# Kernel optimization log

Hardware: AMD Instinct MI355X
Metric: run time of the kernel (lower is better)

Reference implementation:

```python
import jax, jax.numpy as jnp
import numpy as np

NUM_LAYERS = 6
D_MODEL = 256
N_HEADS = 8
N_LEVELS = 4
N_POINTS = 4
D_FFN = 1024
HEAD_DIM = D_MODEL // N_HEADS
B = 2
NQ = 1600
SPATIAL = np.array([[64, 64], [32, 32], [16, 16], [8, 8]], dtype=np.int64)  # (H_l, W_l)
LEVEL_START = np.concatenate([[0], np.cumsum(SPATIAL.prod(1))[:-1]]).astype(np.int64)
S_TOTAL = int(SPATIAL.prod(1).sum())  # 5440


def layer_norm(x, g, b, eps=1e-5):
    mu = x.mean(-1, keepdims=True)
    var = ((x - mu) ** 2).mean(-1, keepdims=True)
    return (x - mu) * jax.lax.rsqrt(var + eps) * g + b


def mha(q, k, v, wq, bq, wk, bk, wv, bv, wo, bo):
    # torch nn.MultiheadAttention math (dropout=eval identity)
    Bb, N, d = q.shape
    def proj(x, w, bias):
        return (x @ w.T + bias).reshape(Bb, -1, N_HEADS, HEAD_DIM).transpose(0, 2, 1, 3)
    qh, kh, vh = proj(q, wq, bq), proj(k, wk, bk), proj(v, wv, bv)
    scores = jnp.einsum('bhqd,bhkd->bhqk', qh, kh) / np.float32(np.sqrt(HEAD_DIM))
    attn = jax.nn.softmax(scores, axis=-1)
    out = jnp.einsum('bhqk,bhkd->bhqd', attn, vh).transpose(0, 2, 1, 3).reshape(Bb, N, d)
    return out @ wo.T + bo


def ms_deform_attn(query, ref_points, src, w_off, b_off, w_attn, b_attn, w_val, b_val, w_out, b_out):
    Bb, Nq, d = query.shape
    value = (src @ w_val.T + b_val).reshape(Bb, -1, N_HEADS, HEAD_DIM)  # [B,S,H,D]
    off = (query @ w_off.T + b_off).reshape(Bb, Nq, N_HEADS, N_LEVELS, N_POINTS, 2)
    aw = (query @ w_attn.T + b_attn).reshape(Bb, Nq, N_HEADS, N_LEVELS * N_POINTS)
    aw = jax.nn.softmax(aw, -1).reshape(Bb, Nq, N_HEADS, N_LEVELS, N_POINTS)
    # offset normalizer is (W_l, H_l)
    norm = jnp.asarray(SPATIAL[:, ::-1].copy(), dtype=query.dtype)  # [L,2]
    loc = ref_points[:, :, None, :, None, :] + off / norm[None, None, None, :, None, :]
    out = jnp.zeros((Bb, Nq, N_HEADS, HEAD_DIM), query.dtype)
    for l in range(N_LEVELS):
        Hl, Wl = int(SPATIAL[l, 0]), int(SPATIAL[l, 1])
        s0 = int(LEVEL_START[l])
        v_l = value[:, s0:s0 + Hl * Wl].transpose(0, 2, 1, 3)  # [B,H,S_l,D]
        loc_l = loc[:, :, :, l]  # [B,Nq,H,P,2]
        # grid_sample bilinear, align_corners=False, padding zeros
        x = loc_l[..., 0] * Wl - 0.5
        y = loc_l[..., 1] * Hl - 0.5
        x0 = jnp.floor(x)
        y0 = jnp.floor(y)
        wx1 = x - x0
        wy1 = y - y0
        samp = jnp.zeros((Bb, Nq, N_HEADS, N_POINTS, HEAD_DIM), query.dtype)
        for dy, wy in ((0, 1.0 - wy1), (1, wy1)):
            for dx, wx in ((0, 1.0 - wx1), (1, wx1)):
                xi = x0 + dx
                yi = y0 + dy
                valid = ((xi >= 0) & (xi <= Wl - 1) & (yi >= 0) & (yi <= Hl - 1)).astype(query.dtype)
                xi_c = jnp.clip(xi, 0, Wl - 1).astype(jnp.int32)
                yi_c = jnp.clip(yi, 0, Hl - 1).astype(jnp.int32)
                idx = (yi_c * Wl + xi_c).transpose(0, 2, 1, 3).reshape(Bb, N_HEADS, Nq * N_POINTS)
                g = jnp.take_along_axis(v_l, idx[..., None], axis=2)  # [B,H,Nq*P,D]
                g = g.reshape(Bb, N_HEADS, Nq, N_POINTS, HEAD_DIM).transpose(0, 2, 1, 3, 4)
                samp = samp + g * (wx * wy * valid)[..., None]
        out = out + (samp * aw[:, :, :, l, :, None]).sum(3)
    return out.reshape(Bb, Nq, d) @ w_out.T + b_out


def decoder_forward(tgt, query_pos, reference_points, src, params):
    out = tgt
    for i in range(NUM_LAYERS):
        p = {k: v[i] for k, v in params.items()}
        q = out + query_pos
        t2 = mha(q, q, out, p['sa_w_q'], p['sa_b_q'], p['sa_w_k'], p['sa_b_k'],
                 p['sa_w_v'], p['sa_b_v'], p['sa_w_o'], p['sa_b_o'])
        out = layer_norm(out + t2, p['ln2_g'], p['ln2_b'])
        t2 = ms_deform_attn(out + query_pos, reference_points, src,
                            p['ca_w_off'], p['ca_b_off'], p['ca_w_attn'], p['ca_b_attn'],
                            p['ca_w_val'], p['ca_b_val'], p['ca_w_out'], p['ca_b_out'])
        out = out + t2
        out = layer_norm(out, p['ln1_g'], p['ln1_b'])
        t2 = jax.nn.relu(out @ p['ffn_w1'].T + p['ffn_b1']) @ p['ffn_w2'].T + p['ffn_b2']
        out = layer_norm(out + t2, p['ln3_g'], p['ln3_b'])
    return out


PARAM_NAMES = ['sa_w_q', 'sa_b_q', 'sa_w_k', 'sa_b_k', 'sa_w_v', 'sa_b_v', 'sa_w_o', 'sa_b_o',
               'ln2_g', 'ln2_b',
               'ca_w_off', 'ca_b_off', 'ca_w_attn', 'ca_b_attn', 'ca_w_val', 'ca_b_val',
               'ca_w_out', 'ca_b_out', 'ln1_g', 'ln1_b',
               'ffn_w1', 'ffn_b1', 'ffn_w2', 'ffn_b2', 'ln3_g', 'ln3_b']


def setup_inputs() -> dict:
    key = jax.random.key(0)
    ks = jax.random.split(key, 64)
    d = D_MODEL
    HLP = N_HEADS * N_LEVELS * N_POINTS
    shapes = {
        'sa_w_q': (d, d), 'sa_b_q': (d,), 'sa_w_k': (d, d), 'sa_b_k': (d,),
        'sa_w_v': (d, d), 'sa_b_v': (d,), 'sa_w_o': (d, d), 'sa_b_o': (d,),
        'ca_w_off': (HLP * 2, d), 'ca_b_off': (HLP * 2,),
        'ca_w_attn': (HLP, d), 'ca_b_attn': (HLP,),
        'ca_w_val': (d, d), 'ca_b_val': (d,),
        'ca_w_out': (d, d), 'ca_b_out': (d,),
        'ffn_w1': (D_FFN, d), 'ffn_b1': (D_FFN,),
        'ffn_w2': (d, D_FFN), 'ffn_b2': (D_FFN * 0 + d,) if False else (d,),
    }
    inp = {}
    inp['tgt'] = jax.random.normal(ks[0], (B, NQ, d), jnp.float32)
    inp['query_pos'] = jax.random.normal(ks[1], (B, NQ, d), jnp.float32)
    inp['reference_points'] = jax.random.uniform(ks[2], (B, NQ, N_LEVELS, 2), jnp.float32)
    inp['src'] = jax.random.normal(ks[3], (B, S_TOTAL, d), jnp.float32)
    i = 4
    for name in PARAM_NAMES:
        if name.startswith('ln'):
            if name.endswith('_g'):
                inp[name] = jnp.ones((NUM_LAYERS, d), jnp.float32)
            else:
                inp[name] = jnp.zeros((NUM_LAYERS, d), jnp.float32)
        else:
            shp = (NUM_LAYERS,) + shapes[name]
            inp[name] = jax.random.normal(ks[i], shp, jnp.float32) * 0.02
            i += 1
    inp['src_spatial_shapes'] = jnp.asarray(SPATIAL)
    inp['src_level_start_index'] = jnp.asarray(LEVEL_START)
    return inp


def reference(tgt, query_pos, reference_points, src,
              sa_w_q, sa_b_q, sa_w_k, sa_b_k, sa_w_v, sa_b_v, sa_w_o, sa_b_o,
              ln2_g, ln2_b,
              ca_w_off, ca_b_off, ca_w_attn, ca_b_attn, ca_w_val, ca_b_val,
              ca_w_out, ca_b_out, ln1_g, ln1_b,
              ffn_w1, ffn_b1, ffn_w2, ffn_b2, ln3_g, ln3_b,
              src_spatial_shapes, src_level_start_index):
    params = dict(zip(PARAM_NAMES, (sa_w_q, sa_b_q, sa_w_k, sa_b_k, sa_w_v, sa_b_v, sa_w_o, sa_b_o,
                                    ln2_g, ln2_b, ca_w_off, ca_b_off, ca_w_attn, ca_b_attn,
                                    ca_w_val, ca_b_val, ca_w_out, ca_b_out, ln1_g, ln1_b,
                                    ffn_w1, ffn_b1, ffn_w2, ffn_b2, ln3_g, ln3_b)))
    return decoder_forward(tgt, query_pos, reference_points, src, params)
```

## Files before the change

### kernel.cpp

```cpp
#include <hip/hip_runtime.h>

#define D_MODEL   256
#define NQ        1600
#define BATCH     2
#define NHEAD     8
#define HDIM      32
#define S_TOTAL   5440
#define D_FFN     1024
#define NUM_LAYERS 6

#define M_Q   (BATCH * NQ)
#define M_V   (BATCH * S_TOTAL)
#define ROW_ELEMS ((size_t)M_Q * D_MODEL)

using short8  = __attribute__((ext_vector_type(8))) short;
using floatx4 = __attribute__((ext_vector_type(4))) float;

__device__ __forceinline__ ushort f2bf(float f) {
    union { float f; unsigned u; } x; x.f = f;
    unsigned r = (x.u + 0x7fffu + ((x.u >> 16) & 1u)) >> 16;
    return (ushort)r;
}
__device__ __forceinline__ float bf2f(ushort b) {
    union { unsigned u; float f; } x; x.u = ((unsigned)b) << 16;
    return x.f;
}

struct GSeg {
    const ushort* A;
    const ushort* W;
    const float*  bias;
    void*         C;
    int           ldc;
    int           mode;
    float         scale;
};
struct GArgs { GSeg s[16]; };

__global__ __launch_bounds__(256) void gemm_multi(GArgs args, int M, int K)
{
    const GSeg sg = args.s[blockIdx.y];
    __shared__ ushort Al[64][40];
    __shared__ ushort Bl[64][40];
    const int tid  = threadIdx.x;
    const int bm   = blockIdx.x * 64;
    const int lr   = tid >> 2;
    const int lc   = tid & 3;
    const int wave = tid >> 6;
    const int lane = tid & 63;
    const int mo   = (wave & 1) * 32;
    const int no   = (wave >> 1) * 32;
    const int row16 = lane & 15;
    const int quad  = lane >> 4;

    floatx4 acc[2][2] = {};

    const ushort* aG = sg.A + (size_t)(bm + lr) * K + lc * 8;
    const ushort* wG = sg.W + (size_t)lr * K + lc * 8;

    for (int k0 = 0; k0 < K; k0 += 32) {
        __syncthreads();
        *(short8*)&Al[lr][lc * 8] = *(const short8*)(aG + k0);
        *(short8*)&Bl[lr][lc * 8] = *(const short8*)(wG + k0);
        __syncthreads();
        short8 af0 = *(const short8*)&Al[mo + row16][quad * 8];
        short8 af1 = *(const short8*)&Al[mo + 16 + row16][quad * 8];
        short8 bf0 = *(const short8*)&Bl[no + row16][quad * 8];
        short8 bf1 = *(const short8*)&Bl[no + 16 + row16][quad * 8];
        acc[0][0] = __builtin_amdgcn_mfma_f32_16x16x32_bf16(af0, bf0, acc[0][0], 0, 0, 0);
        acc[0][1] = __builtin_amdgcn_mfma_f32_16x16x32_bf16(af0, bf1, acc[0][1], 0, 0, 0);
        acc[1][0] = __builtin_amdgcn_mfma_f32_16x16x32_bf16(af1, bf0, acc[1][0], 0, 0, 0);
        acc[1][1] = __builtin_amdgcn_mfma_f32_16x16x32_bf16(af1, bf1, acc[1][1], 0, 0, 0);
    }

#pragma unroll
    for (int mi = 0; mi < 2; ++mi)
#pragma unroll
        for (int ni = 0; ni < 2; ++ni) {
            const int col = no + ni * 16 + row16;
            const float bv = sg.bias[col];
            if (sg.mode == 3) {
                const int rowb = bm + mo + mi * 16 + quad * 4;
                const int b    = rowb / NQ;
                const int mloc = rowb - b * NQ;
                ushort4 st;
                st.x = f2bf((acc[mi][ni][0] + bv) * sg.scale);
                st.y = f2bf((acc[mi][ni][1] + bv) * sg.scale);
                st.z = f2bf((acc[mi][ni][2] + bv) * sg.scale);
                st.w = f2bf((acc[mi][ni][3] + bv) * sg.scale);
                *(ushort4*)((ushort*)sg.C + (size_t)b * (256 * NQ) + (size_t)col * NQ + mloc) = st;
            } else {
#pragma unroll
                for (int r = 0; r < 4; ++r) {
                    const int row = bm + mo + mi * 16 + quad * 4 + r;
                    float v = (acc[mi][ni][r] + bv) * sg.scale;
                    if (sg.mode == 0)
                        ((float*)sg.C)[(size_t)row * sg.ldc + col] = v;
                    else if (sg.mode == 1)
                        ((ushort*)sg.C)[(size_t)row * sg.ldc + col] = f2bf(fmaxf(v, 0.f));
                    else
                        ((ushort*)sg.C)[(size_t)row * sg.ldc + col] = f2bf(v);
                }
            }
        }
}

__global__ __launch_bounds__(256) void attn_mfma(const ushort* __restrict__ Qh,
                                                 const ushort* __restrict__ Kh,
                                                 const ushort* __restrict__ Vt,
                                                 ushort* __restrict__ Oh)
{
    const int bh = blockIdx.x;
    const int h  = bh & 7, b = bh >> 3;
    const int qbase = blockIdx.y * 64;
    const int tid  = threadIdx.x;
    const int wave = tid >> 6, lane = tid & 63;
    const int lr   = lane & 15, quad = lane >> 4;

    __shared__ ushort Kl[64][40];
    __shared__ ushort Vl[32][72];
    __shared__ ushort Pl[4][16][72];

    const short8 qf = *(const short8*)(Qh + (size_t)(b * NQ + qbase + wave * 16 + lr) * 256 + h * 32 + quad * 8);

    float mrow[4] = {-1e30f, -1e30f, -1e30f, -1e30f};
    float lsum[4] = {0.f, 0.f, 0.f, 0.f};
    floatx4 accO[2] = {};
    const floatx4 zero = {0.f, 0.f, 0.f, 0.f};

    const int krow = tid >> 2, kchk = tid & 3;
    const int vrow = tid >> 3, vchk = tid & 7;
    const ushort* Kgb = Kh + (size_t)b * NQ * 256 + h * 32;
    const ushort* Vgb = Vt + (size_t)bh * 32 * NQ;

    for (int k0 = 0; k0 < NQ; k0 += 64) {
        __syncthreads();
        *(short8*)&Kl[krow][kchk * 8] = *(const short8*)(Kgb + (size_t)(k0 + krow) * 256 + kchk * 8);
        *(short8*)&Vl[vrow][vchk * 8] = *(const short8*)(Vgb + (size_t)vrow * NQ + k0 + vchk * 8);
        __syncthreads();

        floatx4 s[4];
#pragma unroll
        for (int cb = 0; cb < 4; ++cb) {
            short8 kf = *(const short8*)&Kl[cb * 16 + lr][quad * 8];
            s[cb] = __builtin_amdgcn_mfma_f32_16x16x32_bf16(qf, kf, zero, 0, 0, 0);
        }
        float corr[4];
#pragma unroll
        for (int r = 0; r < 4; ++r) {
            float mx = fmaxf(fmaxf(s[0][r], s[1][r]), fmaxf(s[2][r], s[3][r]));
            mx = fmaxf(mx, __shfl_xor(mx, 1));
            mx = fmaxf(mx, __shfl_xor(mx, 2));
            mx = fmaxf(mx, __shfl_xor(mx, 4));
            mx = fmaxf(mx, __shfl_xor(mx, 8));
            const float mnew = fmaxf(mrow[r], mx);
            corr[r] = __expf(mrow[r] - mnew);
            mrow[r] = mnew;
        }
        float rsum[4] = {0.f, 0.f, 0.f, 0.f};
#pragma unroll
        for (int cb = 0; cb < 4; ++cb)
#pragma unroll
            for (int r = 0; r < 4; ++r) {
                const float p = __expf(s[cb][r] - mrow[r]);
                s[cb][r] = p;
                rsum[r] += p;
            }
#pragma unroll
        for (int r = 0; r < 4; ++r) {
            float t = rsum[r];
            t += __shfl_xor(t, 1);
            t += __shfl_xor(t, 2);
            t += __shfl_xor(t, 4);
            t += __shfl_xor(t, 8);
            lsum[r] = lsum[r] * corr[r] + t;
            accO[0][r] *= corr[r];
            accO[1][r] *= corr[r];
        }
#pragma unroll
        for (int cb = 0; cb < 4; ++cb)
#pragma unroll
            for (int r = 0; r < 4; ++r)
                Pl[wave][quad * 4 + r][cb * 16 + lr] = f2bf(s[cb][r]);
        __syncthreads();
#pragma unroll
        for (int kc = 0; kc < 2; ++kc) {
            short8 pf = *(const short8*)&Pl[wave][lr][kc * 32 + quad * 8];
            short8 v0 = *(const short8*)&Vl[lr][kc * 32 + quad * 8];
            short8 v1 = *(const short8*)&Vl[16 + lr][kc * 32 + quad * 8];
            accO[0] = __builtin_amdgcn_mfma_f32_16x16x32_bf16(pf, v0, accO[0], 0, 0, 0);
            accO[1] = __builtin_amdgcn_mfma_f32_16x16x32_bf16(pf, v1, accO[1], 0, 0, 0);
        }
    }

    ushort* orow = Oh + (size_t)(b * NQ + qbase + wave * 16) * 256 + h * 32;
#pragma unroll
    for (int r = 0; r < 4; ++r) {
        const float inv = 1.f / lsum[r];
        const int q = quad * 4 + r;
        orow[(size_t)q * 256 + lr]      = f2bf(accO[0][r] * inv);
        orow[(size_t)q * 256 + 16 + lr] = f2bf(accO[1][r] * inv);
    }
}

struct CvtSeg { const float* in; ushort* out; int n4; };
struct CvtArgs { CvtSeg seg[11]; };

__global__ __launch_bounds__(256) void convert_kernel(CvtArgs args)
{
    const CvtSeg sg = args.seg[blockIdx.y];
    const int i = blockIdx.x * 256 + threadIdx.x;
    if (i < sg.n4) {
        float4 v = ((const float4*)sg.in)[i];
        ushort4 o;
        o.x = f2bf(v.x); o.y = f2bf(v.y); o.z = f2bf(v.z); o.w = f2bf(v.w);
        ((ushort4*)sg.out)[i] = o;
    }
}

__global__ __launch_bounds__(256) void init_out_kernel(const float* __restrict__ tgt,
                                                       const float* __restrict__ qpos,
                                                       float* __restrict__ out,
                                                       ushort* __restrict__ out_h,
                                                       ushort* __restrict__ qadd_h, int n4)
{
    const int i = blockIdx.x * 256 + threadIdx.x;
    if (i < n4) {
        float4 v = ((const float4*)tgt)[i];
        float4 p = ((const float4*)qpos)[i];
        ((float4*)out)[i] = v;
        ushort4 o, qa;
        o.x = f2bf(v.x); o.y = f2bf(v.y); o.z = f2bf(v.z); o.w = f2bf(v.w);
        qa.x = f2bf(v.x + p.x); qa.y = f2bf(v.y + p.y);
        qa.z = f2bf(v.z + p.z); qa.w = f2bf(v.w + p.w);
        ((ushort4*)out_h)[i] = o;
        ((ushort4*)qadd_h)[i] = qa;
    }
}

__global__ __launch_bounds__(256) void residual_ln_kernel(const float* __restrict__ x,
                                                          const float* __restrict__ t2,
                                                          const float* __restrict__ g,
                                                          const float* __restrict__ bt,
                                                          const float* __restrict__ qpos,
                                                          float* __restrict__ outp,
                                                          ushort* __restrict__ outp_h,
                                                          ushort* __restrict__ qadd_h)
{
    const int row = blockIdx.x;
    const int c = threadIdx.x;
    const size_t idx = (size_t)row * D_MODEL + c;
    float v = x[idx] + t2[idx];

    float s = v, s2 = v * v;
#pragma unroll
    for (int off = 32; off; off >>= 1) {
        s  += __shfl_xor(s,  off);
        s2 += __shfl_xor(s2, off);
    }
    __shared__ float ws[4], ws2[4];
    const int wid = c >> 6;
    if ((c & 63) == 0) { ws[wid] = s; ws2[wid] = s2; }
    __syncthreads();
    const float tot  = ws[0] + ws[1] + ws[2] + ws[3];
    const float tot2 = ws2[0] + ws2[1] + ws2[2] + ws2[3];
    const float mu  = tot * (1.f / 256.f);
    const float var = tot2 * (1.f / 256.f) - mu * mu;
    const float r = (v - mu) * rsqrtf(var + 1e-5f) * g[c] + bt[c];
    outp[idx] = r;
    outp_h[idx] = f2bf(r);
    qadd_h[idx] = f2bf(r + qpos[idx]);
}

__global__ __launch_bounds__(256) void sample_kernel(const ushort* __restrict__ value,
                                                     const float* __restrict__ off,
                                                     const float* __restrict__ aw,
                                                     const float* __restrict__ ref,
                                                     ushort* __restrict__ outp_h)
{
    const int bq = blockIdx.x;
    const int b  = bq / NQ;
    const int h  = threadIdx.x >> 5;
    const int c  = threadIdx.x & 31;

    const float* offrow = off + (size_t)bq * 256 + h * 32;
    const float* awrow  = aw  + (size_t)bq * 128 + h * 16;
    const float* refrow = ref + (size_t)bq * 8;

    float w16[16];
    {
        float mx = -1e30f;
#pragma unroll
        for (int i = 0; i < 16; ++i) { w16[i] = awrow[i]; mx = fmaxf(mx, w16[i]); }
        float sum = 0.f;
#pragma unroll
        for (int i = 0; i < 16; ++i) { w16[i] = __expf(w16[i] - mx); sum += w16[i]; }
        const float inv = 1.f / sum;
#pragma unroll
        for (int i = 0; i < 16; ++i) w16[i] *= inv;
    }

    const int HL[4]  = {64, 32, 16, 8};
    const int WLv[4] = {64, 32, 16, 8};
    const int S0[4]  = {0, 4096, 5120, 5376};

    float acc = 0.f;
#pragma unroll
    for (int l = 0; l < 4; ++l) {
        const int Hl = HL[l], Wl = WLv[l];
        const float rx = refrow[l * 2 + 0];
        const float ry = refrow[l * 2 + 1];
        const size_t lvl_base = ((size_t)b * S_TOTAL + S0[l]);
#pragma unroll
        for (int p = 0; p < 4; ++p) {
            const float ox = offrow[l * 8 + p * 2 + 0];
            const float oy = offrow[l * 8 + p * 2 + 1];
            const float w  = w16[l * 4 + p];
            const float locx = rx + ox / (float)Wl;
            const float locy = ry + oy / (float)Hl;
            const float x = locx * (float)Wl - 0.5f;
            const float y = locy * (float)Hl - 0.5f;
            const float x0f = floorf(x), y0f = floorf(y);
            const float wx1 = x - x0f, wy1 = y - y0f;
            const int x0 = (int)x0f, y0 = (int)y0f;
#pragma unroll
            for (int dy = 0; dy < 2; ++dy) {
                const int yi = y0 + dy;
                const float wy = dy ? wy1 : (1.f - wy1);
                const bool vy = (yi >= 0) && (yi <= Hl - 1);
                const int yc = min(max(yi, 0), Hl - 1);
#pragma unroll
                for (int dx = 0; dx < 2; ++dx) {
                    const int xi = x0 + dx;
                    const float wx = dx ? wx1 : (1.f - wx1);
                    const bool vx = (xi >= 0) && (xi <= Wl - 1);
                    const int xc = min(max(xi, 0), Wl - 1);
                    const float g = bf2f(value[((lvl_base + (size_t)yc * Wl + xc)) * 256 + h * 32 + c]);
                    acc += (vx && vy) ? g * (wx * wy * w) : 0.f;
                }
            }
        }
    }
    outp_h[(size_t)bq * D_MODEL + h * 32 + c] = f2bf(acc);
}

extern "C" void kernel_launch(void* const* d_in, const int* in_sizes, int n_in,
                              void* d_out, int out_size, void* d_ws, size_t ws_size,
                              hipStream_t stream)
{
    const float* tgt  = (const float*)d_in[0];
    const float* qpos = (const float*)d_in[1];
    const float* refp = (const float*)d_in[2];
    const float* src  = (const float*)d_in[3];

    float* bufT   = (float*)d_ws;
    float* bufOff = bufT   + ROW_ELEMS;
    float* bufAw  = bufOff + ROW_ELEMS;

    ushort* out_h   = (ushort*)(bufAw + (size_t)M_Q * 128);
    ushort* qadd_h  = out_h   + ROW_ELEMS;
    ushort* bufX_h  = qadd_h  + ROW_ELEMS;
    ushort* bufQh   = bufX_h  + ROW_ELEMS;
    ushort* bufKh   = bufQh   + ROW_ELEMS;
    ushort* bufVt   = bufKh   + ROW_ELEMS;
    ushort* bufF_h  = bufVt   + ROW_ELEMS;
    ushort* bufVal  = bufF_h  + (size_t)M_Q * D_FFN;
    ushort* src_h   = bufVal  + (size_t)M_V * D_MODEL;
    ushort* wpool   = src_h   + (size_t)M_V * D_MODEL;

    ushort* wq_h    = wpool;
    ushort* wk_h    = wq_h    + 393216;
    ushort* wv_h    = wk_h    + 393216;
    ushort* wo_h    = wv_h    + 393216;
    ushort* woff_h  = wo_h    + 393216;
    ushort* wattn_h = woff_h  + 393216;
    ushort* wval_h  = wattn_h + 196608;
    ushort* wout_h  = wval_h  + 393216;
    ushort* w1_h    = wout_h  + 393216;
    ushort* w2_h    = w1_h    + 1572864;

    float* out = (float*)d_out;

    CvtArgs ca;
    ca.seg[0]  = { src,                    src_h,   (int)((size_t)M_V * D_MODEL / 4) };
    ca.seg[1]  = { (const float*)d_in[4],  wq_h,    393216 / 4 };
    ca.seg[2]  = { (const float*)d_in[6],  wk_h,    393216 / 4 };
    ca.seg[3]  = { (const float*)d_in[8],  wv_h,    393216 / 4 };
    ca.seg[4]  = { (const float*)d_in[10], wo_h,    393216 / 4 };
    ca.seg[5]  = { (const float*)d_in[14], woff_h,  393216 / 4 };
    ca.seg[6]  = { (const float*)d_in[16], wattn_h, 196608 / 4 };
    ca.seg[7]  = { (const float*)d_in[18], wval_h,  393216 / 4 };
    ca.seg[8]  = { (const float*)d_in[20], wout_h,  393216 / 4 };
    ca.seg[9]  = { (const float*)d_in[24], w1_h,    1572864 / 4 };
    ca.seg[10] = { (const float*)d_in[26], w2_h,    1572864 / 4 };
    convert_kernel<<<dim3(2720, 11), 256, 0, stream>>>(ca);

    init_out_kernel<<<800, 256, 0, stream>>>(tgt, qpos, out, out_h, qadd_h, (int)(ROW_ELEMS / 4));

    const float QSCALE = 0.1767766952966369f;

    for (int l = 0; l < NUM_LAYERS; ++l) {
        const float* sa_b_q    = (const float*)d_in[5]  + (size_t)l * 256;
        const float* sa_b_k    = (const float*)d_in[7]  + (size_t)l * 256;
        const float* sa_b_v    = (const float*)d_in[9]  + (size_t)l * 256;
        const float* sa_b_o    = (const float*)d_in[11] + (size_t)l * 256;
        const float* ln2_g     = (const float*)d_in[12] + (size_t)l * 256;
        const float* ln2_b     = (const float*)d_in[13] + (size_t)l * 256;
        const float* ca_b_off  = (const float*)d_in[15] + (size_t)l * 256;
        const float* ca_b_attn = (const float*)d_in[17] + (size_t)l * 128;
        const float* ca_b_val  = (const float*)d_in[19] + (size_t)l * 256;
        const float* ca_b_out  = (const float*)d_in[21] + (size_t)l * 256;
        const float* ln1_g     = (const float*)d_in[22] + (size_t)l * 256;
        const float* ln1_b     = (const float*)d_in[23] + (size_t)l * 256;
        const float* ffn_b1    = (const float*)d_in[25] + (size_t)l * 1024;
        const float* ffn_b2    = (const float*)d_in[27] + (size_t)l * 256;
        const float* ln3_g     = (const float*)d_in[28] + (size_t)l * 256;
        const float* ln3_b     = (const float*)d_in[29] + (size_t)l * 256;

        const ushort* wq = wq_h    + (size_t)l * 65536;
        const ushort* wk = wk_h    + (size_t)l * 65536;
        const ushort* wv = wv_h    + (size_t)l * 65536;
        const ushort* wo = wo_h    + (size_t)l * 65536;
        const ushort* wf = woff_h  + (size_t)l * 65536;
        const ushort* wa = wattn_h + (size_t)l * 32768;
        const ushort* wl = wval_h  + (size_t)l * 65536;
        const ushort* wu = wout_h  + (size_t)l * 65536;
        const ushort* w1 = w1_h    + (size_t)l * 262144;
        const ushort* w2 = w2_h    + (size_t)l * 262144;

        GArgs ga;

        for (int i = 0; i < 4; ++i) {
            ga.s[i]     = { qadd_h, wq + (size_t)i * 64 * 256, sa_b_q + i * 64, bufQh + i * 64, 256, 2, QSCALE };
            ga.s[4 + i] = { qadd_h, wk + (size_t)i * 64 * 256, sa_b_k + i * 64, bufKh + i * 64, 256, 2, 1.f };
            ga.s[8 + i] = { out_h,  wv + (size_t)i * 64 * 256, sa_b_v + i * 64, bufVt + (size_t)i * 64 * NQ, 256, 3, 1.f };
        }
        gemm_multi<<<dim3(M_Q / 64, 12), 256, 0, stream>>>(ga, M_Q, 256);

        attn_mfma<<<dim3(16, NQ / 64), 256, 0, stream>>>(bufQh, bufKh, bufVt, bufX_h);

        for (int i = 0; i < 4; ++i)
            ga.s[i] = { bufX_h, wo + (size_t)i * 64 * 256, sa_b_o + i * 64, bufT + i * 64, 256, 0, 1.f };
        gemm_multi<<<dim3(M_Q / 64, 4), 256, 0, stream>>>(ga, M_Q, 256);

        residual_ln_kernel<<<M_Q, 256, 0, stream>>>(out, bufT, ln2_g, ln2_b, qpos, out, out_h, qadd_h);

        for (int i = 0; i < 4; ++i)
            ga.s[i] = { qadd_h, wf + (size_t)i * 64 * 256, ca_b_off + i * 64, bufOff + i * 64, 256, 0, 1.f };
        for (int i = 0; i < 2; ++i)
            ga.s[4 + i] = { qadd_h, wa + (size_t)i * 64 * 256, ca_b_attn + i * 64, bufAw + i * 64, 128, 0, 1.f };
        gemm_multi<<<dim3(M_Q / 64, 6), 256, 0, stream>>>(ga, M_Q, 256);

        for (int i = 0; i < 4; ++i)
            ga.s[i] = { src_h, wl + (size_t)i * 64 * 256, ca_b_val + i * 64, bufVal + i * 64, 256, 2, 1.f };
        gemm_multi<<<dim3(M_V / 64, 4), 256, 0, stream>>>(ga, M_V, 256);

        sample_kernel<<<M_Q, 256, 0, stream>>>(bufVal, bufOff, bufAw, refp, bufX_h);

        for (int i = 0; i < 4; ++i)
            ga.s[i] = { bufX_h, wu + (size_t)i * 64 * 256, ca_b_out + i * 64, bufT + i * 64, 256, 0, 1.f };
        gemm_multi<<<dim3(M_Q / 64, 4), 256, 0, stream>>>(ga, M_Q, 256);

        residual_ln_kernel<<<M_Q, 256, 0, stream>>>(out, bufT, ln1_g, ln1_b, qpos, out, out_h, qadd_h);

        for (int i = 0; i < 16; ++i)
            ga.s[i] = { out_h, w1 + (size_t)i * 64 * 256, ffn_b1 + i * 64, bufF_h + i * 64, 1024, 1, 1.f };
        gemm_multi<<<dim3(M_Q / 64, 16), 256, 0, stream>>>(ga, M_Q, 256);

        for (int i = 0; i < 4; ++i)
            ga.s[i] = { bufF_h, w2 + (size_t)i * 64 * 1024, ffn_b2 + i * 64, bufT + i * 64, 256, 0, 1.f };
        gemm_multi<<<dim3(M_Q / 64, 4), 256, 0, stream>>>(ga, M_Q, 1024);

        residual_ln_kernel<<<M_Q, 256, 0, stream>>>(out, bufT, ln3_g, ln3_b, qpos, out, out_h, qadd_h);
    }

    (void)in_sizes; (void)n_in; (void)out_size; (void)ws_size;
}
```

Baseline: 1.068 ms.

## Fuse value projection into QKV GEMM launch and drop LDS staging in attention

The deformable-attention value projection over src is folded into the same multi-segment GEMM launch as the self-attention Q/K/V projections. A per-segment M-block count lets blocks beyond a segment's rows exit early. This removes one launch per layer and lets the larger value GEMM overlap with the smaller QKV work. Separately, the flash-attention kernel now reads K and V fragments straight from global memory instead of staging them in LDS, removing two block barriers per tile but giving up shared reuse of the K/V tiles across the four waves.

```diff
diff --git a/kernel.cpp b/kernel.cpp
--- a/kernel.cpp
+++ b/kernel.cpp
@@ -33,13 +33,15 @@
     void*         C;
     int           ldc;
     int           mode;
+    int           mblk;
     float         scale;
 };
 struct GArgs { GSeg s[16]; };
 
-__global__ __launch_bounds__(256) void gemm_multi(GArgs args, int M, int K)
+__global__ __launch_bounds__(256) void gemm_multi(GArgs args, int K)
 {
     const GSeg sg = args.s[blockIdx.y];
+    if ((int)blockIdx.x >= sg.mblk) return;
     __shared__ ushort Al[64][40];
     __shared__ ushort Bl[64][40];
     const int tid  = threadIdx.x;
@@ -112,37 +114,28 @@
 {
     const int bh = blockIdx.x;
     const int h  = bh & 7, b = bh >> 3;
-    const int qbase = blockIdx.y * 64;
     const int tid  = threadIdx.x;
     const int wave = tid >> 6, lane = tid & 63;
     const int lr   = lane & 15, quad = lane >> 4;
-
-    __shared__ ushort Kl[64][40];
-    __shared__ ushort Vl[32][72];
+    const int q0   = blockIdx.y * 64 + wave * 16;
+
     __shared__ ushort Pl[4][16][72];
 
-    const short8 qf = *(const short8*)(Qh + (size_t)(b * NQ + qbase + wave * 16 + lr) * 256 + h * 32 + quad * 8);
+    const ushort* Kb = Kh + (size_t)b * NQ * 256 + h * 32;
+    const ushort* Vb = Vt + (size_t)bh * 32 * NQ;
+
+    const short8 qf = *(const short8*)(Qh + (size_t)(b * NQ + q0 + lr) * 256 + h * 32 + quad * 8);
 
     float mrow[4] = {-1e30f, -1e30f, -1e30f, -1e30f};
     float lsum[4] = {0.f, 0.f, 0.f, 0.f};
     floatx4 accO[2] = {};
     const floatx4 zero = {0.f, 0.f, 0.f, 0.f};
 
-    const int krow = tid >> 2, kchk = tid & 3;
-    const int vrow = tid >> 3, vchk = tid & 7;
-    const ushort* Kgb = Kh + (size_t)b * NQ * 256 + h * 32;
-    const ushort* Vgb = Vt + (size_t)bh * 32 * NQ;
-
     for (int k0 = 0; k0 < NQ; k0 += 64) {
-        __syncthreads();
-        *(short8*)&Kl[krow][kchk * 8] = *(const short8*)(Kgb + (size_t)(k0 + krow) * 256 + kchk * 8);
-        *(short8*)&Vl[vrow][vchk * 8] = *(const short8*)(Vgb + (size_t)vrow * NQ + k0 + vchk * 8);
-        __syncthreads();
-
         floatx4 s[4];
 #pragma unroll
         for (int cb = 0; cb < 4; ++cb) {
-            short8 kf = *(const short8*)&Kl[cb * 16 + lr][quad * 8];
+            const short8 kf = *(const short8*)(Kb + (size_t)(k0 + cb * 16 + lr) * 256 + quad * 8);
             s[cb] = __builtin_amdgcn_mfma_f32_16x16x32_bf16(qf, kf, zero, 0, 0, 0);
         }
         float corr[4];
@@ -182,18 +175,17 @@
 #pragma unroll
             for (int r = 0; r < 4; ++r)
                 Pl[wave][quad * 4 + r][cb * 16 + lr] = f2bf(s[cb][r]);
-        __syncthreads();
 #pragma unroll
         for (int kc = 0; kc < 2; ++kc) {
-            short8 pf = *(const short8*)&Pl[wave][lr][kc * 32 + quad * 8];
-            short8 v0 = *(const short8*)&Vl[lr][kc * 32 + quad * 8];
-            short8 v1 = *(const short8*)&Vl[16 + lr][kc * 32 + quad * 8];
+            const short8 pf = *(const short8*)&Pl[wave][lr][kc * 32 + quad * 8];
+            const short8 v0 = *(const short8*)(Vb + (size_t)lr * NQ + k0 + kc * 32 + quad * 8);
+            const short8 v1 = *(const short8*)(Vb + (size_t)(16 + lr) * NQ + k0 + kc * 32 + quad * 8);
             accO[0] = __builtin_amdgcn_mfma_f32_16x16x32_bf16(pf, v0, accO[0], 0, 0, 0);
             accO[1] = __builtin_amdgcn_mfma_f32_16x16x32_bf16(pf, v1, accO[1], 0, 0, 0);
         }
     }
 
-    ushort* orow = Oh + (size_t)(b * NQ + qbase + wave * 16) * 256 + h * 32;
+    ushort* orow = Oh + (size_t)(b * NQ + q0) * 256 + h * 32;
 #pragma unroll
     for (int r = 0; r < 4; ++r) {
         const float inv = 1.f / lsum[r];
@@ -398,6 +390,8 @@
     init_out_kernel<<<800, 256, 0, stream>>>(tgt, qpos, out, out_h, qadd_h, (int)(ROW_ELEMS / 4));
 
     const float QSCALE = 0.1767766952966369f;
+    const int MB_Q = M_Q / 64;
+    const int MB_V = M_V / 64;
 
     for (int l = 0; l < NUM_LAYERS; ++l) {
         const float* sa_b_q    = (const float*)d_in[5]  + (size_t)l * 256;
@@ -431,45 +425,42 @@
         GArgs ga;
 
         for (int i = 0; i < 4; ++i) {
-            ga.s[i]     = { qadd_h, wq + (size_t)i * 64 * 256, sa_b_q + i * 64, bufQh + i * 64, 256, 2, QSCALE };
-            ga.s[4 + i] = { qadd_h, wk + (size_t)i * 64 * 256, sa_b_k + i * 64, bufKh + i * 64, 256, 2, 1.f };
-            ga.s[8 + i] = { out_h,  wv + (size_t)i * 64 * 256, sa_b_v + i * 64, bufVt + (size_t)i * 64 * NQ, 256, 3, 1.f };
-        }
-        gemm_multi<<<dim3(M_Q / 64, 12), 256, 0, stream>>>(ga, M_Q, 256);
+            ga.s[i]      = { qadd_h, wq + (size_t)i * 64 * 256, sa_b_q + i * 64, bufQh + i * 64, 256, 2, MB_Q, QSCALE };
+            ga.s[4 + i]  = { qadd_h, wk + (size_t)i * 64 * 256, sa_b_k + i * 64, bufKh + i * 64, 256, 2, MB_Q, 1.f };
+            ga.s[8 + i]  = { out_h,  wv + (size_t)i * 64 * 256, sa_b_v + i * 64, bufVt + (size_t)i * 64 * NQ, 256, 3, MB_Q, 1.f };
+            ga.s[12 + i] = { src_h,  wl + (size_t)i * 64 * 256, ca_b_val + i * 64, bufVal + i * 64, 256, 2, MB_V, 1.f };
+        }
+        gemm_multi<<<dim3(MB_V, 16), 256, 0, stream>>>(ga, 256);
 
         attn_mfma<<<dim3(16, NQ / 64), 256, 0, stream>>>(bufQh, bufKh, bufVt, bufX_h);
 
         for (int i = 0; i < 4; ++i)
-            ga.s[i] = { bufX_h, wo + (size_t)i * 64 * 256, sa_b_o + i * 64, bufT + i * 64, 256, 0, 1.f };
-        gemm_multi<<<dim3(M_Q / 64, 4), 256, 0, stream>>>(ga, M_Q, 256);
+            ga.s[i] = { bufX_h, wo + (size_t)i * 64 * 256, sa_b_o + i * 64, bufT + i * 64, 256, 0, MB_Q, 1.f };
+        gemm_multi<<<dim3(MB_Q, 4), 256, 0, stream>>>(ga, 256);
 
         residual_ln_kernel<<<M_Q, 256, 0, stream>>>(out, bufT, ln2_g, ln2_b, qpos, out, out_h, qadd_h);
 
         for (int i = 0; i < 4; ++i)
-            ga.s[i] = { qadd_h, wf + (size_t)i * 64 * 256, ca_b_off + i * 64, bufOff + i * 64, 256, 0, 1.f };
+            ga.s[i] = { qadd_h, wf + (size_t)i * 64 * 256, ca_b_off + i * 64, bufOff + i * 64, 256, 0, MB_Q, 1.f };
         for (int i = 0; i < 2; ++i)
-            ga.s[4 + i] = { qadd_h, wa + (size_t)i * 64 * 256, ca_b_attn + i * 64, bufAw + i * 64, 128, 0, 1.f };
-        gemm_multi<<<dim3(M_Q / 64, 6), 256, 0, stream>>>(ga, M_Q, 256);
+            ga.s[4 + i] = { qadd_h, wa + (size_t)i * 64 * 256, ca_b_attn + i * 64, bufAw + i * 64, 128, 0, MB_Q, 1.f };
+        gemm_multi<<<dim3(MB_Q, 6), 256, 0, stream>>>(ga, 256);
+
+        sample_kernel<<<M_Q, 256, 0, stream>>>(bufVal, bufOff, bufAw, refp, bufX_h);
 
         for (int i = 0; i < 4; ++i)
-            ga.s[i] = { src_h, wl + (size_t)i * 64 * 256, ca_b_val + i * 64, bufVal + i * 64, 256, 2, 1.f };
-        gemm_multi<<<dim3(M_V / 64, 4), 256, 0, stream>>>(ga, M_V, 256);
-
-        sample_kernel<<<M_Q, 256, 0, stream>>>(bufVal, bufOff, bufAw, refp, bufX_h);
+            ga.s[i] = { bufX_h, wu + (size_t)i * 64 * 256, ca_b_out + i * 64, bufT + i * 64, 256, 0, MB_Q, 1.f };
+        gemm_multi<<<dim3(MB_Q, 4), 256, 0, stream>>>(ga, 256);
+
+        residual_ln_kernel<<<M_Q, 256, 0, stream>>>(out, bufT, ln1_g, ln1_b, qpos, out, out_h, qadd_h);
+
+        for (int i = 0; i < 16; ++i)
+            ga.s[i] = { out_h, w1 + (size_t)i * 64 * 256, ffn_b1 + i * 64, bufF_h + i * 64, 1024, 1, MB_Q, 1.f };
+        gemm_multi<<<dim3(MB_Q, 16), 256, 0, stream>>>(ga, 256);
 
         for (int i = 0; i < 4; ++i)
-            ga.s[i] = { bufX_h, wu + (size_t)i * 64 * 256, ca_b_out + i * 64, bufT + i * 64, 256, 0, 1.f };
-        gemm_multi<<<dim3(M_Q / 64, 4), 256, 0, stream>>>(ga, M_Q, 256);
-
-        residual_ln_kernel<<<M_Q, 256, 0, stream>>>(out, bufT, ln1_g, ln1_b, qpos, out, out_h, qadd_h);
-
-        for (int i = 0; i < 16; ++i)
-            ga.s[i] = { out_h, w1 + (size_t)i * 64 * 256, ffn_b1 + i * 64, bufF_h + i * 64, 1024, 1, 1.f };
-        gemm_multi<<<dim3(M_Q / 64, 16), 256, 0, stream>>>(ga, M_Q, 256);
-
-        for (int i = 0; i < 4; ++i)
-            ga.s[i] = { bufF_h, w2 + (size_t)i * 64 * 1024, ffn_b2 + i * 64, bufT + i * 64, 256, 0, 1.f };
-        gemm_multi<<<dim3(M_Q / 64, 4), 256, 0, stream>>>(ga, M_Q, 1024);
+            ga.s[i] = { bufF_h, w2 + (size_t)i * 64 * 1024, ffn_b2 + i * 64, bufT + i * 64, 256, 0, MB_Q, 1.f };
+        gemm_multi<<<dim3(MB_Q, 4), 256, 0, stream>>>(ga, 1024);
 
         residual_ln_kernel<<<M_Q, 256, 0, stream>>>(out, bufT, ln3_g, ln3_b, qpos, out, out_h, qadd_h);
     }
```

New measurement: 1.051 ms. Within noise of the previous version (-1.7%).
